# Kernel optimization log

Hardware: AMD Instinct MI355X
Metric: run time of the kernel (lower is better)

Reference implementation:

```python
import jax, jax.numpy as jnp
import numpy as np

B, C, H, W_SP = 16, 128, 112, 112  # C doubles as nb_steps (time axis)
KH = 3
TAU_MEM = 1e-3
TAU_SYN = 1e-3
TIME_STEP = 1e-3
ALPHA = float(np.exp(-TIME_STEP / TAU_SYN))
BETA = float(np.exp(-TIME_STEP / TAU_MEM))


def setup_inputs() -> dict:
    key = jax.random.key(0)
    k1, k2 = jax.random.split(key)
    x = jax.random.normal(k1, (B, C, H, W_SP), dtype=jnp.float32)
    # kaiming_uniform_(a=0, mode='fan_in', nonlinearity='linear'): bound = sqrt(3) * 1/sqrt(fan_in)
    fan_in = C * KH * KH
    bound = float(np.sqrt(3.0 / fan_in))
    W = jax.random.uniform(k2, (C, C, KH, KH), minval=-bound, maxval=bound, dtype=jnp.float32)
    b = jnp.zeros((C,), dtype=jnp.float32)
    return {"x": x, "W": W, "b": b}


def reference(x, W, b):
    # Conv2d(in_channel, in_channel, kernel=3, stride=1, padding=1)
    y = jax.lax.conv_general_dilated(
        x, W, window_strides=(1, 1), padding=((1, 1), (1, 1)),
        dimension_numbers=("NCHW", "OIHW", "NCHW")) + b[None, :, None, None]
    conv_shape = y.shape
    Bsz, T = y.shape[0], y.shape[1]  # T == nb_steps (channel axis reused as time)
    X = y.reshape(Bsz, T, -1)  # (B, T, H*W)
    # FFT of leakage kernels: l = alpha^t, k = beta^t * (1 - beta)
    t = jnp.arange(T, dtype=jnp.float32)
    l = jnp.power(jnp.float32(ALPHA), t)
    k = jnp.power(jnp.float32(BETA), t) * (1.0 - jnp.float32(BETA))
    fft_l_k = jnp.fft.rfft(l, n=2 * T) * jnp.fft.rfft(k, n=2 * T)  # (T+1,)
    # Parallel leaky integration via linear (causal) convolution in frequency domain
    fft_X = jnp.fft.rfft(X, n=2 * T, axis=1)  # (B, T+1, H*W) complex
    mem = jnp.fft.irfft(fft_X * fft_l_k[None, :, None], n=2 * T, axis=1)[:, :T]
    return mem.reshape(conv_shape)
```

## Files before the change

kernel.cpp:

```cpp
#include <hip/hip_runtime.h>

typedef __attribute__((ext_vector_type(8))) short s16x8;
typedef __attribute__((ext_vector_type(8))) unsigned short u16x8;
typedef __attribute__((ext_vector_type(4))) float f32x4;

#define ALPHA_F 0.36787944117144233f
#define BETA_F  0.36787944117144233f
#define OMB_F   0.63212055882855767f

#define XS_STRIDE 36
#define YS_STRIDE 130

__device__ __forceinline__ unsigned short f2bf(float f){
  union { float f; unsigned int u; } v; v.f = f;
  unsigned int u = v.u;
  return (unsigned short)((u + 0x7FFFu + ((u >> 16) & 1u)) >> 16);
}
__device__ __forceinline__ float bf2f(unsigned short s){
  union { unsigned int u; float f; } v; v.u = ((unsigned int)s) << 16;
  return v.f;
}

__global__ __launch_bounds__(256) void reorder_w(const float* __restrict__ W,
                                                 unsigned short* __restrict__ Wr){
  int f = blockIdx.x * 256 + threadIdx.x;
  if (f >= 9*128*128) return;
  int cil = f & 31;
  int co  = (f >> 5) & 127;
  int cic = (f >> 12) & 3;
  int pos = f >> 14;
  int ci  = (cic << 5) | cil;
  Wr[f] = f2bf(W[(co*128 + ci)*9 + pos]);
}

__global__ __launch_bounds__(256) void x_to_cl(const float* __restrict__ x,
                                               unsigned short* __restrict__ xcl){
  __shared__ unsigned short ls[112*129];
  const int tid = threadIdx.x;
  const int b = blockIdx.x / 112, h = blockIdx.x % 112;
  const float* xp = x + (size_t)b*1605632 + h*112;
  const int q = tid & 31;
  const int cih = tid >> 5;
  if (q < 28){
    #pragma unroll
    for (int p = 0; p < 16; ++p){
      int ci = (p << 3) + cih;
      float4 v = *(const float4*)(xp + ci*12544 + (q << 2));
      int w0 = q << 2;
      ls[(w0  )*129 + ci] = f2bf(v.x);
      ls[(w0+1)*129 + ci] = f2bf(v.y);
      ls[(w0+2)*129 + ci] = f2bf(v.z);
      ls[(w0+3)*129 + ci] = f2bf(v.w);
    }
  }
  __syncthreads();
  unsigned short* op = xcl + (size_t)(b*112 + h) * (112*128);
  for (int u = tid; u < 112*16; u += 256){
    int pix = u >> 4, cp = u & 15;
    const unsigned short* lr = ls + pix*129 + (cp << 3);
    u16x8 v;
    #pragma unroll
    for (int j = 0; j < 8; ++j) v[j] = lr[j];
    *(u16x8*)(op + (pix << 7) + (cp << 3)) = v;
  }
}

__global__ __launch_bounds__(256, 3) void conv_lif(
    const unsigned short* __restrict__ xcl,
    const unsigned short* __restrict__ Wr,
    const float* __restrict__ bias,
    float* __restrict__ out)
{
  __shared__ unsigned short sm[128*YS_STRIDE];
  const int tid  = threadIdx.x;
  const int lane = tid & 63;
  const int wid  = tid >> 6;
  const int wm   = wid & 1;
  const int wn   = wid >> 1;
  const int l15  = lane & 15;
  const int quad = lane >> 4;
  const int bz = blockIdx.z;
  const int h0 = blockIdx.y * 8, w0 = blockIdx.x * 16;

  f32x4 acc[4][4];
  #pragma unroll
  for (int i=0;i<4;i++)
    #pragma unroll
    for (int j=0;j<4;j++) acc[i][j] = (f32x4){0.f,0.f,0.f,0.f};

  const unsigned short* xb = xcl + (size_t)bz * (112*112*128);

  for (int cic = 0; cic < 4; ++cic){
    __syncthreads();
    const int ci0 = cic << 5;
    #pragma unroll
    for (int it = 0; it < 6; ++it){
      int u = tid + it*256;
      if (u < 1440){
        int posidx = u >> 3, cq = u & 7;
        int r = posidx / 18, c = posidx - r*18;
        int gh = h0 - 1 + r, gw = w0 - 1 + c;
        ushort4 val = make_ushort4(0,0,0,0);
        if (gh >= 0 && gh < 112 && gw >= 0 && gw < 112)
          val = *(const ushort4*)(xb + ((gh*112 + gw) << 7) + ci0 + (cq << 2));
        *(ushort4*)(sm + posidx*XS_STRIDE + (cq << 2)) = val;
      }
    }
    __syncthreads();
    #pragma unroll
    for (int pos = 0; pos < 9; ++pos){
      const int dh = pos/3, dw = pos - dh*3;
      const unsigned short* wb = Wr + (((pos<<2) + cic) << 12) + (wm<<11)
                                    + (l15<<5) + (quad<<3);
      s16x8 af[4];
      #pragma unroll
      for (int mt=0; mt<4; ++mt)
        af[mt] = *(const s16x8*)(wb + (mt<<9));
      #pragma unroll
      for (int nt=0; nt<4; ++nt){
        int rr = (wn<<2) + nt;
        const unsigned short* bp = sm + ((rr+dh)*18 + (l15+dw))*XS_STRIDE + (quad<<3);
        s16x8 bfr = *(const s16x8*)bp;
        #pragma unroll
        for (int mt=0; mt<4; ++mt)
          acc[mt][nt] = __builtin_amdgcn_mfma_f32_16x16x32_bf16(af[mt], bfr, acc[mt][nt], 0, 0, 0);
      }
    }
  }

  __syncthreads();
  #pragma unroll
  for (int mt=0; mt<4; ++mt){
    int cobase = (wm<<6) + (mt<<4) + (quad<<2);
    float4 bv = *(const float4*)(bias + cobase);
    #pragma unroll
    for (int nt=0; nt<4; ++nt){
      int pix = (((wn<<2)+nt)<<4) + l15;
      f32x4 a = acc[mt][nt];
      ushort2 w01, w23;
      w01.x = f2bf(a.x + bv.x);
      w01.y = f2bf(a.y + bv.y);
      w23.x = f2bf(a.z + bv.z);
      w23.y = f2bf(a.w + bv.w);
      unsigned short* yp = sm + pix*YS_STRIDE + cobase;
      *(ushort2*)(yp)     = w01;
      *(ushort2*)(yp + 2) = w23;
    }
  }
  __syncthreads();

  {
    int pix  = tid & 127;
    int half = tid >> 7;
    int r = pix >> 4, c = pix & 15;
    float s = 0.f, m = 0.f;
    float* op = out + (size_t)bz*1605632 + (h0 + r)*112 + (w0 + c);
    const unsigned short* yr = sm + pix*YS_STRIDE;
    int t0    = half ? 48 : 0;
    int tstore= half ? 64 : 0;
    int tend  = half ? 128 : 64;
    for (int t = t0; t < tend; ++t){
      float y = bf2f(yr[t]);
      s = ALPHA_F * s + y;
      m = BETA_F  * m + OMB_F * s;
      if (t >= tstore) op[(size_t)t*12544] = m;
    }
  }
}

extern "C" void kernel_launch(void* const* d_in, const int* in_sizes, int n_in,
                              void* d_out, int out_size, void* d_ws, size_t ws_size,
                              hipStream_t stream){
  const float* x = (const float*)d_in[0];
  const float* W = (const float*)d_in[1];
  const float* b = (const float*)d_in[2];
  float* out = (float*)d_out;
  unsigned short* Wr  = (unsigned short*)d_ws;
  unsigned short* xcl = (unsigned short*)((char*)d_ws + (1 << 20));
  reorder_w<<<576, 256, 0, stream>>>(W, Wr);
  x_to_cl<<<16*112, 256, 0, stream>>>(x, xcl);
  conv_lif<<<dim3(7, 14, 16), 256, 0, stream>>>(xcl, Wr, b, out);
}
```

Before: 297.8 us.

## Double-buffer conv input tiles with register prefetch and pack transpose via shuffles

The conv kernel now precomputes its halo-load addresses, prefetches the next channel chunk into registers, and writes it into a second shared-memory buffer while MFMAs run on the current one. This removes one barrier per chunk and is meant to hide global load latency. The shared stride changes from 36 to 40, which alters the bank pattern for the 16-byte fragment reads. The x_to_cl transpose now packs bf16 pairs with lane shuffles and byte permutes, so it can use 32-bit shared stores and 8-byte reads instead of scalar 16-bit accesses. The cost is more registers in conv_lif, which may hurt occupancy at the launch bound of 3 blocks.

Result: no change. 301.9 us (+1.4%).

```diff
diff --git a/kernel.cpp b/kernel.cpp
--- a/kernel.cpp
+++ b/kernel.cpp
@@ -1,14 +1,14 @@
 #include <hip/hip_runtime.h>
 
 typedef __attribute__((ext_vector_type(8))) short s16x8;
-typedef __attribute__((ext_vector_type(8))) unsigned short u16x8;
 typedef __attribute__((ext_vector_type(4))) float f32x4;
 
 #define ALPHA_F 0.36787944117144233f
 #define BETA_F  0.36787944117144233f
 #define OMB_F   0.63212055882855767f
 
-#define XS_STRIDE 36
+#define XS_STRIDE 40
+#define XS_ELEMS  (180*XS_STRIDE)
 #define YS_STRIDE 130
 
 __device__ __forceinline__ unsigned short f2bf(float f){
@@ -35,33 +35,41 @@
 
 __global__ __launch_bounds__(256) void x_to_cl(const float* __restrict__ x,
                                                unsigned short* __restrict__ xcl){
-  __shared__ unsigned short ls[112*129];
+  __shared__ unsigned int ls32[112*66];
   const int tid = threadIdx.x;
   const int b = blockIdx.x / 112, h = blockIdx.x % 112;
   const float* xp = x + (size_t)b*1605632 + h*112;
-  const int q = tid & 31;
-  const int cih = tid >> 5;
+  const int lane = tid & 63, wid = tid >> 6;
+  const int q = lane >> 1;
+  const int par = lane & 1;
   if (q < 28){
     #pragma unroll
-    for (int p = 0; p < 16; ++p){
-      int ci = (p << 3) + cih;
+    for (int i = 0; i < 16; ++i){
+      int ci = (i << 3) + (wid << 1) + par;
       float4 v = *(const float4*)(xp + ci*12544 + (q << 2));
-      int w0 = q << 2;
-      ls[(w0  )*129 + ci] = f2bf(v.x);
-      ls[(w0+1)*129 + ci] = f2bf(v.y);
-      ls[(w0+2)*129 + ci] = f2bf(v.z);
-      ls[(w0+3)*129 + ci] = f2bf(v.w);
+      unsigned int d01 = (unsigned int)f2bf(v.x) | ((unsigned int)f2bf(v.y) << 16);
+      unsigned int d23 = (unsigned int)f2bf(v.z) | ((unsigned int)f2bf(v.w) << 16);
+      unsigned int o01 = __shfl_xor(d01, 1);
+      unsigned int o23 = __shfl_xor(d23, 1);
+      unsigned int cs = par ? o23 : d01;
+      unsigned int cv = par ? d23 : o01;
+      unsigned int outA = __builtin_amdgcn_perm(cv, cs, 0x05040100u);
+      unsigned int outB = __builtin_amdgcn_perm(cv, cs, 0x07060302u);
+      int wb = (q << 2) + (par << 1);
+      int p  = (i << 2) + wid;
+      ls32[wb*66 + p]       = outA;
+      ls32[(wb+1)*66 + p]   = outB;
     }
   }
   __syncthreads();
   unsigned short* op = xcl + (size_t)(b*112 + h) * (112*128);
-  for (int u = tid; u < 112*16; u += 256){
-    int pix = u >> 4, cp = u & 15;
-    const unsigned short* lr = ls + pix*129 + (cp << 3);
-    u16x8 v;
-    #pragma unroll
-    for (int j = 0; j < 8; ++j) v[j] = lr[j];
-    *(u16x8*)(op + (pix << 7) + (cp << 3)) = v;
+  #pragma unroll
+  for (int it = 0; it < 14; ++it){
+    int idx = it*256 + tid;
+    int pix = idx >> 5, g = idx & 31;
+    const unsigned int* lp = ls32 + pix*66 + (g << 1);
+    uint2 d = *(const uint2*)lp;
+    *(uint2*)(op + (pix << 7) + (g << 2)) = d;
   }
 }
 
@@ -90,23 +98,41 @@
 
   const unsigned short* xb = xcl + (size_t)bz * (112*112*128);
 
+  int s_pos[6], s_valid[6];
+  const unsigned short* s_gp[6];
+  #pragma unroll
+  for (int it = 0; it < 6; ++it){
+    int u = tid + it*256;
+    int posidx = u >> 3, cq = u & 7;
+    int r = posidx / 18, c = posidx - r*18;
+    int gh = h0 - 1 + r, gw = w0 - 1 + c;
+    s_valid[it] = (u < 1440) && (gh >= 0) && (gh < 112) && (gw >= 0) && (gw < 112);
+    s_pos[it]   = posidx*XS_STRIDE + (cq << 2);
+    s_gp[it]    = xb + (((gh*112 + gw) << 7) & 0x7FFFFFF) + (cq << 2);
+  }
+
+  ushort4 r4[6];
+  #define LOADC(cic_) do{ int ci0 = (cic_) << 5; \
+      _Pragma("unroll") \
+      for (int it = 0; it < 6; ++it){ \
+        ushort4 v = make_ushort4(0,0,0,0); \
+        if (s_valid[it]) v = *(const ushort4*)(s_gp[it] + ci0); \
+        r4[it] = v; } }while(0)
+  #define WRITEC(buf_) do{ unsigned short* xw = sm + (buf_)*XS_ELEMS; \
+      _Pragma("unroll") \
+      for (int it = 0; it < 6; ++it){ \
+        int u = tid + it*256; \
+        if (u < 1440) *(ushort4*)(xw + s_pos[it]) = r4[it]; } }while(0)
+
+  LOADC(0); WRITEC(0); LOADC(1);
+
   for (int cic = 0; cic < 4; ++cic){
     __syncthreads();
-    const int ci0 = cic << 5;
-    #pragma unroll
-    for (int it = 0; it < 6; ++it){
-      int u = tid + it*256;
-      if (u < 1440){
-        int posidx = u >> 3, cq = u & 7;
-        int r = posidx / 18, c = posidx - r*18;
-        int gh = h0 - 1 + r, gw = w0 - 1 + c;
-        ushort4 val = make_ushort4(0,0,0,0);
-        if (gh >= 0 && gh < 112 && gw >= 0 && gw < 112)
-          val = *(const ushort4*)(xb + ((gh*112 + gw) << 7) + ci0 + (cq << 2));
-        *(ushort4*)(sm + posidx*XS_STRIDE + (cq << 2)) = val;
-      }
-    }
-    __syncthreads();
+    if (cic < 3){
+      WRITEC((cic+1)&1);
+      if (cic < 2) LOADC(cic+2);
+    }
+    const unsigned short* xs = sm + (cic&1)*XS_ELEMS;
     #pragma unroll
     for (int pos = 0; pos < 9; ++pos){
       const int dh = pos/3, dw = pos - dh*3;
@@ -119,7 +145,7 @@
       #pragma unroll
       for (int nt=0; nt<4; ++nt){
         int rr = (wn<<2) + nt;
-        const unsigned short* bp = sm + ((rr+dh)*18 + (l15+dw))*XS_STRIDE + (quad<<3);
+        const unsigned short* bp = xs + ((rr+dh)*18 + (l15+dw))*XS_STRIDE + (quad<<3);
         s16x8 bfr = *(const s16x8*)bp;
         #pragma unroll
         for (int mt=0; mt<4; ++mt)
```

## Fuse NCHW-to-bf16 layout conversion into conv kernel with double-buffered register gather

Applied to the files above, without the earlier changes.

Drops the separate x_to_cl transpose kernel, so the conv kernel gathers fp32 NCHW input directly, converts it to bf16 and writes it into a double-buffered shared tile. The next channel chunk is gathered while MFMAs for the current chunk run. The warp tiling also changes: each wave now covers 32 output channels by all 8 rows and reuses B-fragment rows across dh through a rotating register window. This removes one kernel launch and the intermediate bf16 tensor round trip through memory. In exchange the strided fp32 gathers (stride 12544 floats per channel) may coalesce poorly, and register pressure rises.

Result: faster. 265.4 us (-10.9%).

```diff
diff --git a/kernel.cpp b/kernel.cpp
--- a/kernel.cpp
+++ b/kernel.cpp
@@ -8,7 +8,7 @@
 #define BETA_F  0.36787944117144233f
 #define OMB_F   0.63212055882855767f
 
-#define XS_STRIDE 36
+#define XS_U16   5760
 #define YS_STRIDE 130
 
 __device__ __forceinline__ unsigned short f2bf(float f){
@@ -33,40 +33,8 @@
   Wr[f] = f2bf(W[(co*128 + ci)*9 + pos]);
 }
 
-__global__ __launch_bounds__(256) void x_to_cl(const float* __restrict__ x,
-                                               unsigned short* __restrict__ xcl){
-  __shared__ unsigned short ls[112*129];
-  const int tid = threadIdx.x;
-  const int b = blockIdx.x / 112, h = blockIdx.x % 112;
-  const float* xp = x + (size_t)b*1605632 + h*112;
-  const int q = tid & 31;
-  const int cih = tid >> 5;
-  if (q < 28){
-    #pragma unroll
-    for (int p = 0; p < 16; ++p){
-      int ci = (p << 3) + cih;
-      float4 v = *(const float4*)(xp + ci*12544 + (q << 2));
-      int w0 = q << 2;
-      ls[(w0  )*129 + ci] = f2bf(v.x);
-      ls[(w0+1)*129 + ci] = f2bf(v.y);
-      ls[(w0+2)*129 + ci] = f2bf(v.z);
-      ls[(w0+3)*129 + ci] = f2bf(v.w);
-    }
-  }
-  __syncthreads();
-  unsigned short* op = xcl + (size_t)(b*112 + h) * (112*128);
-  for (int u = tid; u < 112*16; u += 256){
-    int pix = u >> 4, cp = u & 15;
-    const unsigned short* lr = ls + pix*129 + (cp << 3);
-    u16x8 v;
-    #pragma unroll
-    for (int j = 0; j < 8; ++j) v[j] = lr[j];
-    *(u16x8*)(op + (pix << 7) + (cp << 3)) = v;
-  }
-}
-
 __global__ __launch_bounds__(256, 3) void conv_lif(
-    const unsigned short* __restrict__ xcl,
+    const float* __restrict__ x,
     const unsigned short* __restrict__ Wr,
     const float* __restrict__ bias,
     float* __restrict__ out)
@@ -75,67 +43,107 @@
   const int tid  = threadIdx.x;
   const int lane = tid & 63;
   const int wid  = tid >> 6;
-  const int wm   = wid & 1;
-  const int wn   = wid >> 1;
   const int l15  = lane & 15;
   const int quad = lane >> 4;
   const int bz = blockIdx.z;
   const int h0 = blockIdx.y * 8, w0 = blockIdx.x * 16;
 
-  f32x4 acc[4][4];
+  const float* xb = x + (size_t)bz * 1605632;
+
+  int  g_off[3], g_ci0[3];
+  bool g_val[3];
   #pragma unroll
-  for (int i=0;i<4;i++)
+  for (int it = 0; it < 3; ++it){
+    int u = tid + it*256;
+    bool act = (u < 720);
+    int uu = act ? u : 0;
+    int pos = uu >> 2, cq = uu & 3;
+    int row = pos / 18, col = pos - row*18;
+    int gh = h0 - 1 + row, gw = w0 - 1 + col;
+    bool val = act && (gh >= 0) && (gh < 112) && (gw >= 0) && (gw < 112);
+    g_off[it] = val ? (gh*112 + gw) : 0;
+    g_ci0[it] = cq << 3;
+    g_val[it] = val;
+  }
+
+  u16x8 g[3];
+  #define GATHER(cic_) do{ \
+    _Pragma("unroll") \
+    for (int it = 0; it < 3; ++it){ \
+      const float* p = xb + (size_t)(g_ci0[it] + ((cic_) << 5)) * 12544 + g_off[it]; \
+      u16x8 v; \
+      _Pragma("unroll") \
+      for (int k = 0; k < 8; ++k){ \
+        float f = p[(size_t)k * 12544]; \
+        f = g_val[it] ? f : 0.0f; \
+        v[k] = f2bf(f); \
+      } \
+      g[it] = v; \
+    } }while(0)
+
+  #define WBUF(buf_) do{ \
+    unsigned short* xw = sm + (buf_)*XS_U16; \
+    _Pragma("unroll") \
+    for (int it = 0; it < 3; ++it){ \
+      int u = tid + it*256; \
+      if (u < 720) *(u16x8*)(xw + ((u >> 2) << 5) + ((u & 3) << 3)) = g[it]; \
+    } }while(0)
+
+  f32x4 acc[2][8];
+  #pragma unroll
+  for (int i = 0; i < 2; ++i)
     #pragma unroll
-    for (int j=0;j<4;j++) acc[i][j] = (f32x4){0.f,0.f,0.f,0.f};
+    for (int j = 0; j < 8; ++j) acc[i][j] = (f32x4){0.f,0.f,0.f,0.f};
 
-  const unsigned short* xb = xcl + (size_t)bz * (112*112*128);
+  GATHER(0); WBUF(0);
 
   for (int cic = 0; cic < 4; ++cic){
     __syncthreads();
-    const int ci0 = cic << 5;
+    const unsigned short* xs = sm + (cic & 1)*XS_U16;
     #pragma unroll
-    for (int it = 0; it < 6; ++it){
-      int u = tid + it*256;
-      if (u < 1440){
-        int posidx = u >> 3, cq = u & 7;
-        int r = posidx / 18, c = posidx - r*18;
-        int gh = h0 - 1 + r, gw = w0 - 1 + c;
-        ushort4 val = make_ushort4(0,0,0,0);
-        if (gh >= 0 && gh < 112 && gw >= 0 && gw < 112)
-          val = *(const ushort4*)(xb + ((gh*112 + gw) << 7) + ci0 + (cq << 2));
-        *(ushort4*)(sm + posidx*XS_STRIDE + (cq << 2)) = val;
+    for (int dw = 0; dw < 3; ++dw){
+      s16x8 af[3][2];
+      #pragma unroll
+      for (int dh = 0; dh < 3; ++dh){
+        const unsigned short* wp = Wr + ((((dh*3 + dw) << 2) + cic) << 12)
+                                      + (((wid << 5) + l15) << 5) + (quad << 3);
+        af[dh][0] = *(const s16x8*)wp;
+        af[dh][1] = *(const s16x8*)(wp + 512);
       }
+      const unsigned short* bcol = xs + ((l15 + dw) << 5) + (quad << 3);
+      s16x8 R[6];
+      #pragma unroll
+      for (int r = 0; r < 4; ++r) R[r] = *(const s16x8*)(bcol + r*576);
+      #pragma unroll
+      for (int p = 0; p < 4; ++p){
+        if (p < 3){
+          R[(2*p+4) % 6] = *(const s16x8*)(bcol + (2*p+4)*576);
+          R[(2*p+5) % 6] = *(const s16x8*)(bcol + (2*p+5)*576);
+        }
+        #pragma unroll
+        for (int dh = 0; dh < 3; ++dh){
+          #pragma unroll
+          for (int sub = 0; sub < 2; ++sub){
+            int nt = 2*p + sub;
+            s16x8 b = R[(nt + dh) % 6];
+            acc[0][nt] = __builtin_amdgcn_mfma_f32_16x16x32_bf16(af[dh][0], b, acc[0][nt], 0, 0, 0);
+            acc[1][nt] = __builtin_amdgcn_mfma_f32_16x16x32_bf16(af[dh][1], b, acc[1][nt], 0, 0, 0);
+          }
+        }
+      }
+      if (dw == 1 && cic < 3) GATHER(cic+1);
     }
-    __syncthreads();
-    #pragma unroll
-    for (int pos = 0; pos < 9; ++pos){
-      const int dh = pos/3, dw = pos - dh*3;
-      const unsigned short* wb = Wr + (((pos<<2) + cic) << 12) + (wm<<11)
-                                    + (l15<<5) + (quad<<3);
-      s16x8 af[4];
-      #pragma unroll
-      for (int mt=0; mt<4; ++mt)
-        af[mt] = *(const s16x8*)(wb + (mt<<9));
-      #pragma unroll
-      for (int nt=0; nt<4; ++nt){
-        int rr = (wn<<2) + nt;
-        const unsigned short* bp = sm + ((rr+dh)*18 + (l15+dw))*XS_STRIDE + (quad<<3);
-        s16x8 bfr = *(const s16x8*)bp;
-        #pragma unroll
-        for (int mt=0; mt<4; ++mt)
-          acc[mt][nt] = __builtin_amdgcn_mfma_f32_16x16x32_bf16(af[mt], bfr, acc[mt][nt], 0, 0, 0);
-      }
-    }
+    if (cic < 3) WBUF((cic+1) & 1);
   }
 
   __syncthreads();
   #pragma unroll
-  for (int mt=0; mt<4; ++mt){
-    int cobase = (wm<<6) + (mt<<4) + (quad<<2);
+  for (int mt = 0; mt < 2; ++mt){
+    int cobase = (wid << 5) + (mt << 4) + (quad << 2);
     float4 bv = *(const float4*)(bias + cobase);
     #pragma unroll
-    for (int nt=0; nt<4; ++nt){
-      int pix = (((wn<<2)+nt)<<4) + l15;
+    for (int nt = 0; nt < 8; ++nt){
+      int pix = (nt << 4) + l15;
       f32x4 a = acc[mt][nt];
       ushort2 w01, w23;
       w01.x = f2bf(a.x + bv.x);
@@ -156,9 +164,9 @@
     float s = 0.f, m = 0.f;
     float* op = out + (size_t)bz*1605632 + (h0 + r)*112 + (w0 + c);
     const unsigned short* yr = sm + pix*YS_STRIDE;
-    int t0    = half ? 48 : 0;
-    int tstore= half ? 64 : 0;
-    int tend  = half ? 128 : 64;
+    int t0     = half ? 48 : 0;
+    int tstore = half ? 64 : 0;
+    int tend   = half ? 128 : 64;
     for (int t = t0; t < tend; ++t){
       float y = bf2f(yr[t]);
       s = ALPHA_F * s + y;
@@ -166,6 +174,8 @@
       if (t >= tstore) op[(size_t)t*12544] = m;
     }
   }
+  #undef GATHER
+  #undef WBUF
 }
 
 extern "C" void kernel_launch(void* const* d_in, const int* in_sizes, int n_in,
@@ -175,9 +185,7 @@
   const float* W = (const float*)d_in[1];
   const float* b = (const float*)d_in[2];
   float* out = (float*)d_out;
-  unsigned short* Wr  = (unsigned short*)d_ws;
-  unsigned short* xcl = (unsigned short*)((char*)d_ws + (1 << 20));
+  unsigned short* Wr = (unsigned short*)d_ws;
   reorder_w<<<576, 256, 0, stream>>>(W, Wr);
-  x_to_cl<<<16*112, 256, 0, stream>>>(x, xcl);
-  conv_lif<<<dim3(7, 14, 16), 256, 0, stream>>>(xcl, Wr, b, out);
+  conv_lif<<<dim3(7, 14, 16), 256, 0, stream>>>(x, Wr, b, out);
 }
```
